# Performance work log

Measured on AMD Instinct MI355X. Metric: run time of the kernel, lower is better.

The kernel has to match this reference:

```python
import jax, jax.numpy as jnp
import numpy as np

HEADS = 4
EPS_LN = 1e-5
EPS_NORM = 1e-12

def conv1x1(x, w):
    # x: [B,C,T,H,W], w: [O,C] (Conv3d kernel_size=1, no bias)
    return jnp.einsum('oc,bcthw->bothw', w, x)

def dwconv3(x, w):
    # depthwise Conv3d 3x3x3, padding=1; w: [C,1,3,3,3]
    return jax.lax.conv_general_dilated(
        x, w, window_strides=(1, 1, 1), padding='SAME',
        dimension_numbers=('NCDHW', 'OIDHW', 'NCDHW'),
        feature_group_count=x.shape[1])

def layernorm_c(x, w, b):
    # LayerNorm over channel dim (torch LN applied after b c t h w -> b (thw) c)
    m = jnp.mean(x, axis=1, keepdims=True)
    v = jnp.mean(jnp.square(x - m), axis=1, keepdims=True)
    xn = (x - m) * jax.lax.rsqrt(v + EPS_LN)
    return xn * w[None, :, None, None, None] + b[None, :, None, None, None]

def l2norm(x):
    n = jnp.sqrt(jnp.sum(jnp.square(x), axis=-1, keepdims=True))
    return x / jnp.maximum(n, EPS_NORM)

def attention_c(x, qkv_w, qkv_dw_w, proj_w, temperature):
    B, C, T, H, W = x.shape
    qkv = dwconv3(conv1x1(x, qkv_w), qkv_dw_w)  # [B,3C,T,H,W]
    q, k, v = jnp.split(qkv, 3, axis=1)
    def to_heads(a):
        return a.reshape(B, HEADS, C // HEADS, T * H * W)  # b head c (thw)
    q, k, v = to_heads(q), to_heads(k), to_heads(v)
    q = l2norm(q)
    k = l2norm(k)
    # channel attention: [b,h,c,c] score matrix scaled by learnable temperature
    attn = jnp.einsum('bhcn,bhdn->bhcd', q, k) * temperature[None]
    attn = jax.nn.softmax(attn, axis=-1)
    out = jnp.einsum('bhcd,bhdn->bhcn', attn, v)
    out = out.reshape(B, C, T, H, W)
    return conv1x1(out, proj_w)

def feedforward(x, pin_w, ffn_dw_w, pout_w):
    h = conv1x1(x, pin_w)            # [B,2H,T,H,W]
    h = dwconv3(h, ffn_dw_w)
    x1, x2 = jnp.split(h, 2, axis=1)
    g = jax.nn.gelu(x1, approximate=False) * x2
    return conv1x1(g, pout_w)

def setup_inputs() -> dict:
    key = jax.random.key(0)
    ks = jax.random.split(key, 8)
    C, T, H, W = 192, 10, 64, 64
    Hf = int(C * 2.66)  # 510
    s = 0.05
    return {
        'x': jax.random.normal(ks[0], (1, C, T, H, W), jnp.float32),
        'ln1_w': jnp.ones((C,), jnp.float32),
        'ln1_b': jnp.zeros((C,), jnp.float32),
        'qkv_w': jax.random.normal(ks[1], (3 * C, C), jnp.float32) * s,
        'qkv_dw_w': jax.random.normal(ks[2], (3 * C, 1, 3, 3, 3), jnp.float32) * s,
        'proj_w': jax.random.normal(ks[3], (C, C), jnp.float32) * s,
        'temperature': jnp.ones((HEADS, 1, 1), jnp.float32),
        'ln2_w': jnp.ones((C,), jnp.float32),
        'ln2_b': jnp.zeros((C,), jnp.float32),
        'pin_w': jax.random.normal(ks[4], (2 * Hf, C), jnp.float32) * s,
        'ffn_dw_w': jax.random.normal(ks[5], (2 * Hf, 1, 3, 3, 3), jnp.float32) * s,
        'pout_w': jax.random.normal(ks[6], (C, Hf), jnp.float32) * s,
    }

def reference(x, ln1_w, ln1_b, qkv_w, qkv_dw_w, proj_w, temperature,
              ln2_w, ln2_b, pin_w, ffn_dw_w, pout_w):
    y = x + attention_c(layernorm_c(x, ln1_w, ln1_b), qkv_w, qkv_dw_w, proj_w, temperature)
    out = y + feedforward(layernorm_c(y, ln2_w, ln2_b), pin_w, ffn_dw_w, pout_w)
    return out
```

## Files before the change

### kernel.cpp

```cpp
#include <hip/hip_runtime.h>
#include <math.h>

#define NPOS 40960
#define TT 10
#define HH 64
#define WW 64
#define HWP 4096
#define CIN 192
#define C3 576
#define NHEADS 4
#define CHD 48
#define HF 510
#define GNB 80
#define GCHUNK 512

typedef unsigned short u16;
typedef unsigned int   u32;
typedef __bf16 bf16x8 __attribute__((ext_vector_type(8)));
typedef __bf16 bf16x2 __attribute__((ext_vector_type(2)));
typedef float  f32x4  __attribute__((ext_vector_type(4)));
typedef u16    u16x8  __attribute__((ext_vector_type(8)));
typedef u16    u16x4  __attribute__((ext_vector_type(4)));
typedef u32    u32x4  __attribute__((ext_vector_type(4)));
typedef u32    u32x2  __attribute__((ext_vector_type(2)));

__device__ __forceinline__ float b2f(u16 u) {
    return __uint_as_float(((unsigned int)u) << 16);
}
__device__ __forceinline__ u16 f2b(float f) {
    unsigned int i = __float_as_uint(f);
    unsigned int r = (i + 0x7FFFu + ((i >> 16) & 1u)) >> 16;
    return (u16)r;
}
__device__ __forceinline__ u16 f2bh(float f) {
    return __builtin_bit_cast(u16, static_cast<__bf16>(f));
}
__device__ __forceinline__ float gelu_fast(float v) {
    float z = fabsf(v) * 0.70710678118654752f;
    float d = fmaf(0.3275911f, z, 1.0f);
#if __has_builtin(__builtin_amdgcn_rcpf)
    float t = __builtin_amdgcn_rcpf(d);
#else
    float t = 1.0f / d;
#endif
    float p = fmaf(1.061405429f, t, -1.453152027f);
    p = fmaf(p, t, 1.421413741f);
    p = fmaf(p, t, -0.284496736f);
    p = fmaf(p, t, 0.254829592f);
    p = p * t;
    float e = __expf(-z * z);
    float E = fmaf(-p, e, 1.0f);
    return 0.5f * v * (1.0f + copysignf(E, v));
}

__device__ __forceinline__ float dot2bf(u32 a, u32 b, float c) {
#if __has_builtin(__builtin_amdgcn_fdot2_f32_bf16)
    return __builtin_amdgcn_fdot2_f32_bf16(
        __builtin_bit_cast(bf16x2, a), __builtin_bit_cast(bf16x2, b), c, false);
#else
    float a0 = b2f((u16)(a & 0xffffu)), a1 = b2f((u16)(a >> 16));
    float b0 = b2f((u16)(b & 0xffffu)), b1 = b2f((u16)(b >> 16));
    return fmaf(a1, b1, fmaf(a0, b0, c));
#endif
}
__device__ __forceinline__ u32 alignp(u32 hi, u32 lo) {
#if __has_builtin(__builtin_amdgcn_alignbit)
    return __builtin_amdgcn_alignbit(hi, lo, 16);
#else
    return (lo >> 16) | (hi << 16);
#endif
}

__device__ __forceinline__ u32 dpp_prev(u32 v) {
#if __has_builtin(__builtin_amdgcn_update_dpp)
    return (u32)__builtin_amdgcn_update_dpp(0, (int)v, 0x111, 0xF, 0xF, true);
#else
    int l = (int)(threadIdx.x & 63);
    u32 r = __shfl(v, l - 1);
    return ((l & 15) == 0) ? 0u : r;
#endif
}
__device__ __forceinline__ u32 dpp_next(u32 v) {
#if __has_builtin(__builtin_amdgcn_update_dpp)
    return (u32)__builtin_amdgcn_update_dpp(0, (int)v, 0x101, 0xF, 0xF, true);
#else
    int l = (int)(threadIdx.x & 63);
    u32 r = __shfl(v, l + 1);
    return ((l & 15) == 15) ? 0u : r;
#endif
}
__device__ __forceinline__ u32 dpp_prev8(u32 v, bool edge) {
    u32 r = dpp_prev(v);
    return edge ? 0u : r;
}
__device__ __forceinline__ u32 dpp_next8(u32 v, bool edge) {
    u32 r = dpp_next(v);
    return edge ? 0u : r;
}

#define GLD_LDS16(g, l) __builtin_amdgcn_global_load_lds( \
    (const __attribute__((address_space(1))) void*)(g), \
    (__attribute__((address_space(3))) void*)(l), 16, 0, 0)

#define CVT_N1 (640 * 192)
#define CVT_N2 (1024 * 192)
#define CVT_N3 (256 * 512)
__global__ void cvtw_k(const float* __restrict__ qkv_w, const float* __restrict__ pin_w,
                       const float* __restrict__ pout_w,
                       u16* __restrict__ qkv_wb, u16* __restrict__ pin_wb,
                       u16* __restrict__ pout_wb) {
    int idx = blockIdx.x * 256 + threadIdx.x;
    if (idx < CVT_N1) {
        int r = idx / 192, c = idx % 192;
        qkv_wb[idx] = f2bh(r < 576 ? qkv_w[r * 192 + c] : 0.f);
    } else if (idx < CVT_N1 + CVT_N2) {
        int k = idx - CVT_N1;
        int r = k / 192, c = k % 192;
        pin_wb[k] = f2bh(r < 1020 ? pin_w[r * 192 + c] : 0.f);
    } else if (idx < CVT_N1 + CVT_N2 + CVT_N3) {
        int k = idx - CVT_N1 - CVT_N2;
        int r = k / 512, c = k % 512;
        pout_wb[k] = f2bh((r < 192 && c < 510) ? pout_w[r * 510 + c] : 0.f);
    }
}

template<typename InT>
__global__ __launch_bounds__(256) void lnt_k(const InT* __restrict__ X,
                                             const float* __restrict__ w,
                                             const float* __restrict__ b,
                                             u16* __restrict__ Xt) {
    __shared__ float sm[CIN][65];
    __shared__ float ps[4][64], ps2[4][64];
    __shared__ float smean[64], srstd[64];
    __shared__ float sw[CIN], sb[CIN];
    const int tid = threadIdx.x;
    const int n0 = blockIdx.x * 64;
    if (tid < CIN) { sw[tid] = w[tid]; sb[tid] = b[tid]; }
    if constexpr (sizeof(InT) == 4) {
        #pragma unroll
        for (int i = 0; i < 12; ++i) {
            int e = i * 256 + tid;
            int c = e >> 4, p4 = (e & 15) * 4;
            float4 v = *(const float4*)((const float*)X + (size_t)c * NPOS + n0 + p4);
            sm[c][p4 + 0] = v.x; sm[c][p4 + 1] = v.y;
            sm[c][p4 + 2] = v.z; sm[c][p4 + 3] = v.w;
        }
    } else {
        #pragma unroll
        for (int i = 0; i < 6; ++i) {
            int e = i * 256 + tid;
            int c = e >> 3, p8 = (e & 7) * 8;
            u16x8 v = *(const u16x8*)((const u16*)X + (size_t)c * NPOS + n0 + p8);
            #pragma unroll
            for (int j = 0; j < 8; ++j) sm[c][p8 + j] = b2f(v[j]);
        }
    }
    __syncthreads();
    int g = tid >> 6, nn = tid & 63;
    float s = 0.f, s2 = 0.f;
    for (int c = g * 48; c < g * 48 + 48; ++c) {
        float v = sm[c][nn];
        s += v; s2 += v * v;
    }
    ps[g][nn] = s; ps2[g][nn] = s2;
    __syncthreads();
    if (g == 0) {
        float t = ps[0][nn] + ps[1][nn] + ps[2][nn] + ps[3][nn];
        float t2 = ps2[0][nn] + ps2[1][nn] + ps2[2][nn] + ps2[3][nn];
        float m = t / CIN;
        float var = t2 / CIN - m * m;
        smean[nn] = m;
        srstd[nn] = rsqrtf(var + 1e-5f);
    }
    __syncthreads();
    #pragma unroll
    for (int i = 0; i < 6; ++i) {
        int e = i * 256 + tid;
        int nl = e / 24, cg = e % 24;
        int c0 = cg * 8;
        float m = smean[nl], rs_ = srstd[nl];
        u16x8 o;
        #pragma unroll
        for (int j = 0; j < 8; ++j) {
            float v = (sm[c0 + j][nl] - m) * rs_ * sw[c0 + j] + sb[c0 + j];
            o[j] = f2bh(v);
        }
        *(u16x8*)(Xt + (size_t)(n0 + nl) * CIN + c0) = o;
    }
}

__global__ __launch_bounds__(256) void transpose_pad_k(const u16* __restrict__ src,
                                                       u16* __restrict__ dst,
                                                       int CS, int CD) {
    __shared__ float sm[64][65];
    const int tid = threadIdx.x;
    const int n0 = blockIdx.x * 64;
    const int cb = blockIdx.y * 64;
    #pragma unroll
    for (int i = 0; i < 2; ++i) {
        int e = i * 256 + tid;
        int cl = e >> 3, nn8 = (e & 7) * 8;
        int c = cb + cl;
        if (c < CS) {
            u16x8 v = *(const u16x8*)(src + (size_t)c * NPOS + n0 + nn8);
            #pragma unroll
            for (int j = 0; j < 8; ++j) sm[cl][nn8 + j] = b2f(v[j]);
        } else {
            #pragma unroll
            for (int j = 0; j < 8; ++j) sm[cl][nn8 + j] = 0.f;
        }
    }
    __syncthreads();
    #pragma unroll
    for (int i = 0; i < 2; ++i) {
        int e = i * 256 + tid;
        int nl = e >> 3, c0 = (e & 7) * 8;
        u16x8 o;
        #pragma unroll
        for (int j = 0; j < 8; ++j) o[j] = f2bh(sm[c0 + j][nl]);
        *(u16x8*)(dst + (size_t)(n0 + nl) * CD + cb + c0) = o;
    }
}

template<int KP, typename OutT, typename ResT, bool RESID>
__global__ __launch_bounds__(256) void gemm_mfma_k(
    const u16* __restrict__ A, const u16* __restrict__ Bt, int O,
    const ResT* __restrict__ resid, OutT* __restrict__ outp)
{
    constexpr int NT = KP / 32;
    __shared__ u16 As[2][128 * 32];
    __shared__ u16 Bs[2][128 * 32];
    const int tid  = threadIdx.x;
    const int lane = tid & 63;
    const int wv   = tid >> 6;
    const int lo = lane & 15, hi = lane >> 4;
    const int m_blk = blockIdx.y * 128;
    const int n_blk = blockIdx.x * 128;

    int bb0 = (0 * 4 + wv) * 1024 + lane * 16;
    int bb1 = (1 * 4 + wv) * 1024 + lane * 16;
    const int r0 = bb0 >> 6, c80 = (bb0 >> 4) & 3;
    const int r1 = bb1 >> 6, c81 = (bb1 >> 4) & 3;

    auto stage = [&](int buf, int k0) {
        GLD_LDS16(A  + (size_t)(m_blk + r0) * KP + k0 + c80 * 8, (char*)&As[buf][0] + (0 * 4 + wv) * 1024);
        GLD_LDS16(A  + (size_t)(m_blk + r1) * KP + k0 + c81 * 8, (char*)&As[buf][0] + (1 * 4 + wv) * 1024);
        GLD_LDS16(Bt + (size_t)(n_blk + r0) * KP + k0 + c80 * 8, (char*)&Bs[buf][0] + (0 * 4 + wv) * 1024);
        GLD_LDS16(Bt + (size_t)(n_blk + r1) * KP + k0 + c81 * 8, (char*)&Bs[buf][0] + (1 * 4 + wv) * 1024);
    };

    f32x4 acc[4][4];
    const f32x4 zero = {0.f, 0.f, 0.f, 0.f};
    #pragma unroll
    for (int mt = 0; mt < 4; ++mt)
        #pragma unroll
        for (int nt = 0; nt < 4; ++nt) acc[mt][nt] = zero;

    stage(0, 0);
    __syncthreads();

    #pragma unroll
    for (int t = 0; t < NT; ++t) {
        if (t + 1 < NT) stage((t + 1) & 1, (t + 1) * 32);
        const u16* Ab = &As[t & 1][0] + (wv & 1) * 64 * 32;
        const u16* Bb = &Bs[t & 1][0] + (wv >> 1) * 64 * 32;
        bf16x8 a[4], b[4];
        #pragma unroll
        for (int q = 0; q < 4; ++q) {
            a[q] = *(const bf16x8*)(Ab + (q * 16 + lo) * 32 + hi * 8);
            b[q] = *(const bf16x8*)(Bb + (q * 16 + lo) * 32 + hi * 8);
        }
        #pragma unroll
        for (int mt = 0; mt < 4; ++mt)
            #pragma unroll
            for (int nt = 0; nt < 4; ++nt)
                acc[mt][nt] = __builtin_amdgcn_mfma_f32_16x16x32_bf16(
                    a[mt], b[nt], acc[mt][nt], 0, 0, 0);
        __syncthreads();
    }

    const int m_base = m_blk + (wv & 1) * 64;
    const int n_base = n_blk + (wv >> 1) * 64;
    #pragma unroll
    for (int mt = 0; mt < 4; ++mt) {
        #pragma unroll
        for (int r = 0; r < 4; ++r) {
            int m = m_base + mt * 16 + hi * 4 + r;
            if (m < O) {
                size_t rowoff = (size_t)m * NPOS;
                #pragma unroll
                for (int nt = 0; nt < 4; ++nt) {
                    int n = n_base + nt * 16 + lo;
                    float v = acc[mt][nt][r];
                    if (RESID) {
                        if constexpr (sizeof(ResT) == 2) v += b2f(((const u16*)resid)[rowoff + n]);
                        else                             v += ((const float*)resid)[rowoff + n];
                    }
                    if constexpr (sizeof(OutT) == 2) outp[rowoff + n] = (OutT)f2bh(v);
                    else                             outp[rowoff + n] = (OutT)v;
                }
            }
        }
    }
}

__global__ __launch_bounds__(256) void dwconv_k(const u16* __restrict__ in,
                                                u16* __restrict__ outp,
                                                const float* __restrict__ wgt,
                                                float* __restrict__ nrm2)
{
    __shared__ float red[256];
    const int lane = threadIdx.x & 63;
    const int wv   = threadIdx.x >> 6;
    const int c    = blockIdx.x >> 1;
    const int hb   = blockIdx.x & 1;
    const int h    = hb * 32 + wv * 8 + (lane >> 3);
    const int w0c  = (lane & 7) * 8;
    const bool wl0 = (lane & 7) == 0;
    const bool wl7 = (lane & 7) == 7;
    const bool hup = (h > 0), hdn = (h < HH - 1);
    u32 W01[9], W2h[9];
    {
        const float* wc = wgt + c * 27;
        #pragma unroll
        for (int i = 0; i < 9; ++i) {
            float a = wc[i * 3 + 0], b = wc[i * 3 + 1], d = wc[i * 3 + 2];
            W01[i] = (u32)f2b(a) | ((u32)f2b(b) << 16);
            W2h[i] = ((u32)f2b(d)) << 16;
        }
    }
    const u16* base = in   + (size_t)c * (TT * HWP);
    u16*       ob   = outp + (size_t)c * (TT * HWP);

    u32x4 zv = {0u, 0u, 0u, 0u};
    u32x4 ld[3][3];
    auto issue = [&](int ph, int ts) {
        const u16* rp = base + (size_t)ts * HWP + h * WW + w0c;
        ld[ph][0] = hup ? *(const u32x4*)(rp - WW) : zv;
        ld[ph][1] = *(const u32x4*)(rp);
        ld[ph][2] = hdn ? *(const u32x4*)(rp + WW) : zv;
    };

    float acc[3][8];
    #pragma unroll
    for (int o_ = 0; o_ < 3; ++o_)
        #pragma unroll
        for (int j = 0; j < 8; ++j) acc[o_][j] = 0.f;
    float sq = 0.f;

    issue(0, 0);
    issue(1, 1);
    #pragma unroll
    for (int ts = 0; ts < TT; ++ts) {
        const int cb = ts % 3;
        if (ts + 2 < TT) issue((ts + 2) % 3, ts + 2);
        #pragma unroll
        for (int dh = 0; dh < 3; ++dh) {
            u32 P0 = ld[cb][dh][0], P1 = ld[cb][dh][1];
            u32 P2 = ld[cb][dh][2], P3 = ld[cb][dh][3];
            u32 Pm = dpp_prev8(P3, wl0);
            u32 Pp = dpp_next8(P0, wl7);
            u32 S0 = alignp(P0, Pm), S1 = alignp(P1, P0);
            u32 S2 = alignp(P2, P1), S3 = alignp(P3, P2);
            u32 S4 = alignp(Pp, P3);
            #pragma unroll
            for (int tp = 0; tp < 3; ++tp) {
                int o_;
                if (tp == 2) { if (ts < 1) continue; o_ = (ts - 1) % 3; }
                else if (tp == 1) { o_ = ts % 3; }
                else { if (ts + 1 >= TT) continue; o_ = (ts + 1) % 3; }
                const u32 wA = W01[tp * 3 + dh], wB = W2h[tp * 3 + dh];
                float* ap = acc[o_];
                ap[0] = dot2bf(S0, wA, ap[0]); ap[0] = dot2bf(P0, wB, ap[0]);
                ap[1] = dot2bf(P0, wA, ap[1]); ap[1] = dot2bf(S1, wB, ap[1]);
                ap[2] = dot2bf(S1, wA, ap[2]); ap[2] = dot2bf(P1, wB, ap[2]);
                ap[3] = dot2bf(P1, wA, ap[3]); ap[3] = dot2bf(S2, wB, ap[3]);
                ap[4] = dot2bf(S2, wA, ap[4]); ap[4] = dot2bf(P2, wB, ap[4]);
                ap[5] = dot2bf(P2, wA, ap[5]); ap[5] = dot2bf(S3, wB, ap[5]);
                ap[6] = dot2bf(S3, wA, ap[6]); ap[6] = dot2bf(P3, wB, ap[6]);
                ap[7] = dot2bf(P3, wA, ap[7]); ap[7] = dot2bf(S4, wB, ap[7]);
            }
        }
        if (ts >= 1) {
            const int o_ = (ts - 1) % 3;
            u16x8 o;
            #pragma unroll
            for (int j = 0; j < 8; ++j) {
                float v = acc[o_][j];
                sq = fmaf(v, v, sq);
                o[j] = f2bh(v);
            }
            *(u16x8*)(ob + (size_t)(ts - 1) * HWP + h * WW + w0c) = o;
            #pragma unroll
            for (int j = 0; j < 8; ++j) acc[o_][j] = 0.f;
        }
    }
    {
        const int o_ = (TT - 1) % 3;
        u16x8 o;
        #pragma unroll
        for (int j = 0; j < 8; ++j) {
            float v = acc[o_][j];
            sq = fmaf(v, v, sq);
            o[j] = f2bh(v);
        }
        *(u16x8*)(ob + (size_t)(TT - 1) * HWP + h * WW + w0c) = o;
    }
    if (nrm2) {
        red[threadIdx.x] = sq;
        __syncthreads();
        for (int off = 128; off > 0; off >>= 1) {
            if (threadIdx.x < off) red[threadIdx.x] += red[threadIdx.x + off];
            __syncthreads();
        }
        if (threadIdx.x == 0) nrm2[c * 2 + hb] = red[0];
    }
}

__global__ __launch_bounds__(256) void dwconv_glu3_k(const u16* __restrict__ in,
                                                     u16* __restrict__ gout,
                                                     const float* __restrict__ wgt)
{
    const int lane = threadIdx.x & 63;
    const int wv   = threadIdx.x >> 6;
    const int cpr  = blockIdx.x >> 2;
    const int hb   = blockIdx.x & 3;
    const int h    = hb * 16 + wv * 4 + (lane >> 4);
    const int w0c  = (lane & 15) * 4;
    const bool hup = (h > 0), hdn = (h < HH - 1);

    u32 W01[2][9], W2h[2][9];
    #pragma unroll
    for (int ch = 0; ch < 2; ++ch) {
        const float* wc = wgt + (size_t)(cpr + ch * HF) * 27;
        #pragma unroll
        for (int i = 0; i < 9; ++i) {
            float a = wc[i * 3 + 0], b = wc[i * 3 + 1], d = wc[i * 3 + 2];
            W01[ch][i] = (u32)f2b(a) | ((u32)f2b(b) << 16);
            W2h[ch][i] = ((u32)f2b(d)) << 16;
        }
    }
    const u16* base0 = in + (size_t)cpr * (TT * HWP);
    const u16* base1 = in + (size_t)(cpr + HF) * (TT * HWP);
    u16* ob = gout + (size_t)cpr * (TT * HWP);

    u32x2 zv = {0u, 0u};
    u32x2 ld[2][3][3];
    auto issue = [&](int ph, int ts) {
        const u16* rp0 = base0 + (size_t)ts * HWP + h * WW + w0c;
        ld[0][ph][0] = hup ? *(const u32x2*)(rp0 - WW) : zv;
        ld[0][ph][1] = *(const u32x2*)(rp0);
        ld[0][ph][2] = hdn ? *(const u32x2*)(rp0 + WW) : zv;
        const u16* rp1 = base1 + (size_t)ts * HWP + h * WW + w0c;
        ld[1][ph][0] = hup ? *(const u32x2*)(rp1 - WW) : zv;
        ld[1][ph][1] = *(const u32x2*)(rp1);
        ld[1][ph][2] = hdn ? *(const u32x2*)(rp1 + WW) : zv;
    };

    float acc[2][3][4];
    #pragma unroll
    for (int ch = 0; ch < 2; ++ch)
        #pragma unroll
        for (int o_ = 0; o_ < 3; ++o_)
            #pragma unroll
            for (int j = 0; j < 4; ++j) acc[ch][o_][j] = 0.f;

    auto emit = [&](int ots) {
        const int o_ = ots % 3;
        u16x4 o;
        #pragma unroll
        for (int j = 0; j < 4; ++j)
            o[j] = f2bh(gelu_fast(acc[0][o_][j]) * acc[1][o_][j]);
        *(u16x4*)(ob + (size_t)ots * HWP + h * WW + w0c) = o;
        #pragma unroll
        for (int j = 0; j < 4; ++j) { acc[0][o_][j] = 0.f; acc[1][o_][j] = 0.f; }
    };

    issue(0, 0);
    issue(1, 1);
    #pragma unroll
    for (int ts = 0; ts < TT; ++ts) {
        const int cb = ts % 3;
        if (ts + 2 < TT) issue((ts + 2) % 3, ts + 2);
        #pragma unroll
        for (int ch = 0; ch < 2; ++ch) {
            #pragma unroll
            for (int dh = 0; dh < 3; ++dh) {
                u32 P0 = ld[ch][cb][dh][0], P1 = ld[ch][cb][dh][1];
                u32 Pm = dpp_prev(P1);
                u32 Pp = dpp_next(P0);
                u32 S0 = alignp(P0, Pm), S1 = alignp(P1, P0), S2 = alignp(Pp, P1);
                #pragma unroll
                for (int tp = 0; tp < 3; ++tp) {
                    int o_;
                    if (tp == 2) { if (ts < 1) continue; o_ = (ts - 1) % 3; }
                    else if (tp == 1) { o_ = ts % 3; }
                    else { if (ts + 1 >= TT) continue; o_ = (ts + 1) % 3; }
                    const u32 wA = W01[ch][tp * 3 + dh], wB = W2h[ch][tp * 3 + dh];
                    float* ap = acc[ch][o_];
                    ap[0] = dot2bf(S0, wA, ap[0]); ap[0] = dot2bf(P0, wB, ap[0]);
                    ap[1] = dot2bf(P0, wA, ap[1]); ap[1] = dot2bf(S1, wB, ap[1]);
                    ap[2] = dot2bf(S1, wA, ap[2]); ap[2] = dot2bf(P1, wB, ap[2]);
                    ap[3] = dot2bf(P1, wA, ap[3]); ap[3] = dot2bf(S2, wB, ap[3]);
                }
            }
        }
        if (ts >= 1) emit(ts - 1);
    }
    emit(TT - 1);
}

__global__ __launch_bounds__(64) void gram_k(const u16* __restrict__ qkv,
                                             float* __restrict__ part) {
    const int h  = blockIdx.x / GNB;
    const int nb = blockIdx.x % GNB;
    const int lane = threadIdx.x;
    const int lo = lane & 15, hi = lane >> 4;
    const u16* qp = qkv + (size_t)(h * CHD) * NPOS + (size_t)nb * GCHUNK + hi * 8;
    const u16* kp = qkv + (size_t)(CIN + h * CHD) * NPOS + (size_t)nb * GCHUNK + hi * 8;
    f32x4 acc[3][3];
    const f32x4 zero = {0.f, 0.f, 0.f, 0.f};
    #pragma unroll
    for (int mt = 0; mt < 3; ++mt)
        #pragma unroll
        for (int nt = 0; nt < 3; ++nt) acc[mt][nt] = zero;
    #pragma unroll
    for (int ks = 0; ks < GCHUNK; ks += 32) {
        bf16x8 a[3], b[3];
        #pragma unroll
        for (int t = 0; t < 3; ++t) {
            a[t] = *(const bf16x8*)(qp + (size_t)(t * 16 + lo) * NPOS + ks);
            b[t] = *(const bf16x8*)(kp + (size_t)(t * 16 + lo) * NPOS + ks);
        }
        #pragma unroll
        for (int mt = 0; mt < 3; ++mt)
            #pragma unroll
            for (int nt = 0; nt < 3; ++nt)
                acc[mt][nt] = __builtin_amdgcn_mfma_f32_16x16x32_bf16(
                    a[mt], b[nt], acc[mt][nt], 0, 0, 0);
    }
    float* pp = part + (size_t)blockIdx.x * 2304;
    #pragma unroll
    for (int mt = 0; mt < 3; ++mt)
        #pragma unroll
        for (int nt = 0; nt < 3; ++nt)
            #pragma unroll
            for (int r = 0; r < 4; ++r)
                pp[(mt * 16 + hi * 4 + r) * 48 + nt * 16 + lo] = acc[mt][nt][r];
}

__global__ __launch_bounds__(64) void gram_softmax_k(const float* __restrict__ part,
                                                     const float* __restrict__ norm2p,
                                                     const float* __restrict__ temp,
                                                     float* __restrict__ attn) {
    const int row = blockIdx.x;
    const int h = row / CHD, r = row % CHD;
    const int d = threadIdx.x;
    float s = 0.f;
    if (d < CHD) {
        const float* pp = part + (size_t)h * GNB * 2304 + r * 48 + d;
        for (int nb = 0; nb < GNB; ++nb) s += pp[(size_t)nb * 2304];
    }
    float v = -1e30f;
    if (d < CHD) {
        float qn = fmaxf(sqrtf(norm2p[2 * row] + norm2p[2 * row + 1]), 1e-12f);
        int kc = CIN + h * CHD + d;
        float kn = fmaxf(sqrtf(norm2p[2 * kc] + norm2p[2 * kc + 1]), 1e-12f);
        v = temp[h] * s / (qn * kn);
    }
    float mx = v;
    #pragma unroll
    for (int o = 32; o > 0; o >>= 1) mx = fmaxf(mx, __shfl_xor(mx, o));
    float e = (d < CHD) ? expf(v - mx) : 0.f;
    float se = e;
    #pragma unroll
    for (int o = 32; o > 0; o >>= 1) se += __shfl_xor(se, o);
    if (d < CHD) attn[row * CHD + d] = e / se;
}

__global__ void mmat_k(const float* __restrict__ proj_w, const float* __restrict__ attn,
                       u16* __restrict__ Mb) {
    int idx = blockIdx.x * blockDim.x + threadIdx.x;
    if (idx >= 256 * CIN) return;
    int o = idx / CIN, j = idx % CIN;
    float s = 0.f;
    if (o < CIN) {
        int h = j / CHD, d = j % CHD;
        for (int c = 0; c < CHD; ++c)
            s += proj_w[o * CIN + h * CHD + c] * attn[(h * CHD + c) * CHD + d];
    }
    Mb[idx] = f2bh(s);
}

extern "C" void kernel_launch(void* const* d_in, const int* in_sizes, int n_in,
                              void* d_out, int out_size, void* d_ws, size_t ws_size,
                              hipStream_t stream) {
    const float* x       = (const float*)d_in[0];
    const float* ln1w    = (const float*)d_in[1];
    const float* ln1b    = (const float*)d_in[2];
    const float* qkv_w   = (const float*)d_in[3];
    const float* qkv_dw  = (const float*)d_in[4];
    const float* proj_w  = (const float*)d_in[5];
    const float* temp    = (const float*)d_in[6];
    const float* ln2w    = (const float*)d_in[7];
    const float* ln2b    = (const float*)d_in[8];
    const float* pin_w   = (const float*)d_in[9];
    const float* ffn_dw  = (const float*)d_in[10];
    const float* pout_w  = (const float*)d_in[11];
    float* out = (float*)d_out;

    char* wsb = (char*)d_ws;
    size_t off = 0;
    auto alloc = [&](size_t bytes) {
        void* p = wsb + off; off += (bytes + 255) & ~(size_t)255; return p;
    };
    float* norm2p  = (float*)alloc(C3 * 2 * 4);
    float* attn    = (float*)alloc(NHEADS * 2304 * 4);
    float* part    = (float*)alloc((size_t)NHEADS * GNB * 2304 * 4);
    u16*   qkv_wb  = (u16*)alloc((size_t)640 * 192 * 2);
    u16*   pin_wb  = (u16*)alloc((size_t)1024 * 192 * 2);
    u16*   pout_wb = (u16*)alloc((size_t)256 * 512 * 2);
    u16*   M_b     = (u16*)alloc((size_t)256 * 192 * 2);
    u16*   xn1_t   = (u16*)alloc((size_t)NPOS * 192 * 2);
    u16*   yn2_t   = (u16*)alloc((size_t)NPOS * 192 * 2);
    u16*   ybuf    = (u16*)alloc((size_t)CIN * NPOS * 2);
    u16*   regionA = (u16*)alloc((size_t)1024 * NPOS * 2);
    u16*   regionB = (u16*)alloc((size_t)1024 * NPOS * 2);
    u16* qkv_raw  = regionA;
    u16* qkv_conv = regionB;
    u16* h_raw    = regionA;
    u16* g510     = regionB;
    u16* gt       = regionA;
    u16* vt       = xn1_t;

    cvtw_k<<<(CVT_N1 + CVT_N2 + CVT_N3 + 255) / 256, 256, 0, stream>>>(
        qkv_w, pin_w, pout_w, qkv_wb, pin_wb, pout_wb);
    lnt_k<float><<<NPOS / 64, 256, 0, stream>>>(x, ln1w, ln1b, xn1_t);
    gemm_mfma_k<192, u16, float, false><<<dim3(NPOS / 128, 5), 256, 0, stream>>>(
        qkv_wb, xn1_t, C3, nullptr, qkv_raw);
    dwconv_k<<<C3 * 2, 256, 0, stream>>>(qkv_raw, qkv_conv, qkv_dw, norm2p);
    gram_k<<<NHEADS * GNB, 64, 0, stream>>>(qkv_conv, part);
    gram_softmax_k<<<192, 64, 0, stream>>>(part, norm2p, temp, attn);
    mmat_k<<<(256 * CIN + 255) / 256, 256, 0, stream>>>(proj_w, attn, M_b);
    transpose_pad_k<<<dim3(NPOS / 64, 3), 256, 0, stream>>>(
        qkv_conv + (size_t)384 * NPOS, vt, 192, 192);
    gemm_mfma_k<192, u16, float, true><<<dim3(NPOS / 128, 2), 256, 0, stream>>>(
        M_b, vt, CIN, x, ybuf);
    lnt_k<u16><<<NPOS / 64, 256, 0, stream>>>(ybuf, ln2w, ln2b, yn2_t);
    gemm_mfma_k<192, u16, float, false><<<dim3(NPOS / 128, 8), 256, 0, stream>>>(
        pin_wb, yn2_t, 1024, nullptr, h_raw);
    dwconv_glu3_k<<<HF * 4, 256, 0, stream>>>(h_raw, g510, ffn_dw);
    transpose_pad_k<<<dim3(NPOS / 64, 8), 256, 0, stream>>>(g510, gt, HF, 512);
    gemm_mfma_k<512, float, u16, true><<<dim3(NPOS / 128, 2), 256, 0, stream>>>(
        pout_wb, gt, CIN, ybuf, out);
}
```

Baseline: 233.6 us.

## Fuse channel-major transposes into GEMM B-operand staging with swizzled LDS

Removes the two standalone transpose_pad kernels that converted channel-major activations into position-major layout before the V-projection and FFN output GEMMs. A new GEMM variant instead loads B directly from the [K][NPOS] layout, packs pairs of K rows in registers and writes them into LDS with an XOR swizzle, overlapping the global load with MFMA work. The GLU depthwise kernel now zero-fills two padding channels so K can be 512 without a separate pad step. This saves a full read and write of the intermediate tensors, at the cost of register-staged B loads and scattered 32-bit LDS writes instead of direct global-to-LDS copies.

```diff
diff --git a/kernel.cpp b/kernel.cpp
--- a/kernel.cpp
+++ b/kernel.cpp
@@ -189,39 +189,6 @@
     }
 }
 
-__global__ __launch_bounds__(256) void transpose_pad_k(const u16* __restrict__ src,
-                                                       u16* __restrict__ dst,
-                                                       int CS, int CD) {
-    __shared__ float sm[64][65];
-    const int tid = threadIdx.x;
-    const int n0 = blockIdx.x * 64;
-    const int cb = blockIdx.y * 64;
-    #pragma unroll
-    for (int i = 0; i < 2; ++i) {
-        int e = i * 256 + tid;
-        int cl = e >> 3, nn8 = (e & 7) * 8;
-        int c = cb + cl;
-        if (c < CS) {
-            u16x8 v = *(const u16x8*)(src + (size_t)c * NPOS + n0 + nn8);
-            #pragma unroll
-            for (int j = 0; j < 8; ++j) sm[cl][nn8 + j] = b2f(v[j]);
-        } else {
-            #pragma unroll
-            for (int j = 0; j < 8; ++j) sm[cl][nn8 + j] = 0.f;
-        }
-    }
-    __syncthreads();
-    #pragma unroll
-    for (int i = 0; i < 2; ++i) {
-        int e = i * 256 + tid;
-        int nl = e >> 3, c0 = (e & 7) * 8;
-        u16x8 o;
-        #pragma unroll
-        for (int j = 0; j < 8; ++j) o[j] = f2bh(sm[c0 + j][nl]);
-        *(u16x8*)(dst + (size_t)(n0 + nl) * CD + cb + c0) = o;
-    }
-}
-
 template<int KP, typename OutT, typename ResT, bool RESID>
 __global__ __launch_bounds__(256) void gemm_mfma_k(
     const u16* __restrict__ A, const u16* __restrict__ Bt, int O,
@@ -276,6 +243,108 @@
             for (int nt = 0; nt < 4; ++nt)
                 acc[mt][nt] = __builtin_amdgcn_mfma_f32_16x16x32_bf16(
                     a[mt], b[nt], acc[mt][nt], 0, 0, 0);
+        __syncthreads();
+    }
+
+    const int m_base = m_blk + (wv & 1) * 64;
+    const int n_base = n_blk + (wv >> 1) * 64;
+    #pragma unroll
+    for (int mt = 0; mt < 4; ++mt) {
+        #pragma unroll
+        for (int r = 0; r < 4; ++r) {
+            int m = m_base + mt * 16 + hi * 4 + r;
+            if (m < O) {
+                size_t rowoff = (size_t)m * NPOS;
+                #pragma unroll
+                for (int nt = 0; nt < 4; ++nt) {
+                    int n = n_base + nt * 16 + lo;
+                    float v = acc[mt][nt][r];
+                    if (RESID) {
+                        if constexpr (sizeof(ResT) == 2) v += b2f(((const u16*)resid)[rowoff + n]);
+                        else                             v += ((const float*)resid)[rowoff + n];
+                    }
+                    if constexpr (sizeof(OutT) == 2) outp[rowoff + n] = (OutT)f2bh(v);
+                    else                             outp[rowoff + n] = (OutT)v;
+                }
+            }
+        }
+    }
+}
+
+template<int KP, typename OutT, typename ResT, bool RESID>
+__global__ __launch_bounds__(256) void gemm_bt_k(
+    const u16* __restrict__ A, const u16* __restrict__ Bkn, int O,
+    const ResT* __restrict__ resid, OutT* __restrict__ outp)
+{
+    constexpr int NT = KP / 32;
+    __shared__ u16 As[2][128 * 32];
+    __shared__ u16 Bs[2][128 * 32];
+    const int tid  = threadIdx.x;
+    const int lane = tid & 63;
+    const int wv   = tid >> 6;
+    const int lo = lane & 15, hi = lane >> 4;
+    const int m_blk = blockIdx.y * 128;
+    const int n_blk = blockIdx.x * 128;
+
+    int bb0 = (0 * 4 + wv) * 1024 + lane * 16;
+    int bb1 = (1 * 4 + wv) * 1024 + lane * 16;
+    const int r0 = bb0 >> 6, c80 = (bb0 >> 4) & 3;
+    const int r1 = bb1 >> 6, c81 = (bb1 >> 4) & 3;
+    auto stageA = [&](int buf, int k0) {
+        GLD_LDS16(A + (size_t)(m_blk + r0) * KP + k0 + c80 * 8, (char*)&As[buf][0] + (0 * 4 + wv) * 1024);
+        GLD_LDS16(A + (size_t)(m_blk + r1) * KP + k0 + c81 * 8, (char*)&As[buf][0] + (1 * 4 + wv) * 1024);
+    };
+
+    const int kp2 = (tid & 15) * 2;
+    const int nf  = (tid >> 4) * 8;
+    const int kb  = kp2 >> 3;
+    const int klo = kp2 & 7;
+    u16x8 bv0, bv1;
+    auto loadB = [&](int k0) {
+        const u16* sp = Bkn + (size_t)(k0 + kp2) * NPOS + n_blk + nf;
+        bv0 = *(const u16x8*)(sp);
+        bv1 = *(const u16x8*)(sp + NPOS);
+    };
+    auto writeB = [&](int buf) {
+        #pragma unroll
+        for (int i = 0; i < 8; ++i) {
+            int n = nf + i;
+            int idx = n * 32 + ((kb ^ ((n >> 4) & 3)) << 3) + klo;
+            u32 pk = (u32)bv0[i] | ((u32)bv1[i] << 16);
+            *(u32*)&Bs[buf][idx] = pk;
+        }
+    };
+
+    f32x4 acc[4][4];
+    const f32x4 zero = {0.f, 0.f, 0.f, 0.f};
+    #pragma unroll
+    for (int mt = 0; mt < 4; ++mt)
+        #pragma unroll
+        for (int nt = 0; nt < 4; ++nt) acc[mt][nt] = zero;
+
+    stageA(0, 0);
+    loadB(0);
+    writeB(0);
+    __syncthreads();
+
+    #pragma unroll
+    for (int t = 0; t < NT; ++t) {
+        if (t + 1 < NT) { stageA((t + 1) & 1, (t + 1) * 32); loadB((t + 1) * 32); }
+        const u16* Ab = &As[t & 1][0] + (wv & 1) * 64 * 32;
+        const u16* Bb = &Bs[t & 1][0] + (wv >> 1) * 64 * 32;
+        bf16x8 a[4], b[4];
+        #pragma unroll
+        for (int q = 0; q < 4; ++q) {
+            a[q] = *(const bf16x8*)(Ab + (q * 16 + lo) * 32 + hi * 8);
+            b[q] = *(const bf16x8*)(Bb + (q * 16 + lo) * 32 + ((hi ^ (q & 3)) * 8));
+        }
+        #pragma unroll
+        for (int mt = 0; mt < 4; ++mt)
+            #pragma unroll
+            for (int nt = 0; nt < 4; ++nt)
+                acc[mt][nt] = __builtin_amdgcn_mfma_f32_16x16x32_bf16(
+                    a[mt], b[nt], acc[mt][nt], 0, 0, 0);
+        if (t + 1 < NT) writeB((t + 1) & 1);
         __syncthreads();
     }
 
@@ -427,6 +496,14 @@
     const int hb   = blockIdx.x & 3;
     const int h    = hb * 16 + wv * 4 + (lane >> 4);
     const int w0c  = (lane & 15) * 4;
+    u16* ob = gout + (size_t)cpr * (TT * HWP);
+    if (cpr >= HF) {
+        u16x4 z = {0, 0, 0, 0};
+        #pragma unroll
+        for (int ts = 0; ts < TT; ++ts)
+            *(u16x4*)(ob + (size_t)ts * HWP + h * WW + w0c) = z;
+        return;
+    }
     const bool hup = (h > 0), hdn = (h < HH - 1);
 
     u32 W01[2][9], W2h[2][9];
@@ -442,7 +519,6 @@
     }
     const u16* base0 = in + (size_t)cpr * (TT * HWP);
     const u16* base1 = in + (size_t)(cpr + HF) * (TT * HWP);
-    u16* ob = gout + (size_t)cpr * (TT * HWP);
 
     u32x2 zv = {0u, 0u};
     u32x2 ld[2][3][3];
@@ -629,9 +705,7 @@
     u16* qkv_raw  = regionA;
     u16* qkv_conv = regionB;
     u16* h_raw    = regionA;
-    u16* g510     = regionB;
-    u16* gt       = regionA;
-    u16* vt       = xn1_t;
+    u16* g512     = regionB;
 
     cvtw_k<<<(CVT_N1 + CVT_N2 + CVT_N3 + 255) / 256, 256, 0, stream>>>(
         qkv_w, pin_w, pout_w, qkv_wb, pin_wb, pout_wb);
@@ -642,15 +716,12 @@
     gram_k<<<NHEADS * GNB, 64, 0, stream>>>(qkv_conv, part);
     gram_softmax_k<<<192, 64, 0, stream>>>(part, norm2p, temp, attn);
     mmat_k<<<(256 * CIN + 255) / 256, 256, 0, stream>>>(proj_w, attn, M_b);
-    transpose_pad_k<<<dim3(NPOS / 64, 3), 256, 0, stream>>>(
-        qkv_conv + (size_t)384 * NPOS, vt, 192, 192);
-    gemm_mfma_k<192, u16, float, true><<<dim3(NPOS / 128, 2), 256, 0, stream>>>(
-        M_b, vt, CIN, x, ybuf);
+    gemm_bt_k<192, u16, float, true><<<dim3(NPOS / 128, 2), 256, 0, stream>>>(
+        M_b, qkv_conv + (size_t)384 * NPOS, CIN, x, ybuf);
     lnt_k<u16><<<NPOS / 64, 256, 0, stream>>>(ybuf, ln2w, ln2b, yn2_t);
     gemm_mfma_k<192, u16, float, false><<<dim3(NPOS / 128, 8), 256, 0, stream>>>(
         pin_wb, yn2_t, 1024, nullptr, h_raw);
-    dwconv_glu3_k<<<HF * 4, 256, 0, stream>>>(h_raw, g510, ffn_dw);
-    transpose_pad_k<<<dim3(NPOS / 64, 8), 256, 0, stream>>>(g510, gt, HF, 512);
-    gemm_mfma_k<512, float, u16, true><<<dim3(NPOS / 128, 2), 256, 0, stream>>>(
-        pout_wb, gt, CIN, ybuf, out);
-}
+    dwconv_glu3_k<<<(HF + 2) * 4, 256, 0, stream>>>(h_raw, g512, ffn_dw);
+    gemm_bt_k<512, float, u16, true><<<dim3(NPOS / 128, 2), 256, 0, stream>>>(
+        pout_wb, g512, CIN, ybuf, out);
+}
```

Measured after the change: 219.2 us. 6.2% less time.
